# Optimization experiments

Hardware: AMD Instinct MI355X
Metric: run time of the kernel (lower is better)

## Reference

```python
import jax, jax.numpy as jnp
import numpy as np
from jax import lax

B, S = 256, 512
CHAR_NUM, CLASS_NUM, OUTPUT_NUM, WORD_EMBED, H = 10, 10, 64, 32, 128
EPS = 1e-12


def setup_inputs() -> dict:
    key = jax.random.key(0)
    ks = jax.random.split(key, 16)
    def nrm(k, shape, s=0.05):
        return jax.random.normal(k, shape, dtype=jnp.float32) * s
    return {
        "char_ids": jax.random.randint(ks[0], (B, S), 0, CHAR_NUM),
        "word_ids": jax.random.randint(ks[1], (B, S), 0, CHAR_NUM),
        "subject_ids": jax.random.randint(ks[2], (B, 2), 0, S),
        "emb_char": nrm(ks[3], (CHAR_NUM, OUTPUT_NUM)),
        "emb_word": nrm(ks[4], (CHAR_NUM, WORD_EMBED)),
        "Wwc": nrm(ks[5], (WORD_EMBED, OUTPUT_NUM)),
        "bwc": jnp.zeros((OUTPUT_NUM,), jnp.float32),
        "l1_Wx": nrm(ks[6], (OUTPUT_NUM, 4 * H)),
        "l1_Wh": nrm(ks[7], (H, 4 * H)),
        "l1_b": jnp.zeros((4 * H,), jnp.float32),
        "l2_Wx": nrm(ks[8], (H, 4 * H)),
        "l2_Wh": nrm(ks[9], (H, 4 * H)),
        "l2_b": jnp.zeros((4 * H,), jnp.float32),
        "beta_W": nrm(ks[10], (2 * H, H)),
        "beta_b": jnp.zeros((H,), jnp.float32),
        "gamma_W": nrm(ks[11], (2 * H, H)),
        "gamma_b": jnp.zeros((H,), jnp.float32),
        "sub_W": nrm(ks[12], (H, 2)),
        "sub_b": jnp.zeros((2,), jnp.float32),
        "po_W": nrm(ks[13], (H, 2 * CLASS_NUM)),
        "po_b": jnp.zeros((2 * CLASS_NUM,), jnp.float32),
    }


def _lstm_cell(x, h, c, Wx, Wh, b):
    # Keras LSTMCell: gates ordered i, f, g(cell), o
    z = x @ Wx + h @ Wh + b
    i, f, g, o = jnp.split(z, 4, axis=-1)
    c_new = jax.nn.sigmoid(f) * c + jax.nn.sigmoid(i) * jnp.tanh(g)
    h_new = jax.nn.sigmoid(o) * jnp.tanh(c_new)
    return h_new, c_new


def reference(char_ids, word_ids, subject_ids,
              emb_char, emb_word, Wwc, bwc,
              l1_Wx, l1_Wh, l1_b, l2_Wx, l2_Wh, l2_b,
              beta_W, beta_b, gamma_W, gamma_b,
              sub_W, sub_b, po_W, po_b):
    b, s = char_ids.shape
    # NOTE: source passes mask = (char_ids == 0) to the RNN; in Keras, mask True
    # means the step IS processed, so only positions with id==0 update state.
    step_mask = (char_ids == 0)  # [B, S] bool

    emb = emb_char[char_ids] + (emb_word[word_ids] @ Wwc + bwc)  # [B, S, 64]

    def step(carry, inp):
        h1, c1, h2, c2 = carry
        xt, mt = inp  # xt [B, 64], mt [B]
        h1n, c1n = _lstm_cell(xt, h1, c1, l1_Wx, l1_Wh, l1_b)
        h2n, c2n = _lstm_cell(h1n, h2, c2, l2_Wx, l2_Wh, l2_b)
        m = mt[:, None]
        h1 = jnp.where(m, h1n, h1)
        c1 = jnp.where(m, c1n, c1)
        h2 = jnp.where(m, h2n, h2)
        c2 = jnp.where(m, c2n, c2)
        return (h1, c1, h2, c2), h2

    z = jnp.zeros((b, H), emb.dtype)
    _, outs = lax.scan(step, (z, z, z, z),
                       (emb.transpose(1, 0, 2), step_mask.T))
    sent = outs.transpose(1, 0, 2)  # [B, S, 128]

    # vectorized batch_gather (replaces eager numpy per-row loop)
    bidx = jnp.arange(b)
    sub_start = sent[bidx, subject_ids[:, 0]]  # [B, 128]
    sub_end = sent[bidx, subject_ids[:, 1]]    # [B, 128]
    subject = jnp.concatenate([sub_start, sub_end], axis=1)  # [B, 256]

    # conditional layer norm
    beta = subject @ beta_W + beta_b    # [B, 128]
    gamma = subject @ gamma_W + gamma_b
    u = jnp.mean(sent, axis=-1, keepdims=True)
    v = jnp.mean((sent - u) ** 2, axis=-1, keepdims=True)
    xhat = (sent - u) / jnp.sqrt(v + EPS)
    context = gamma[:, None, :] * xhat + beta[:, None, :]  # [B, S, 128]

    # (transformer_encoder LSTM(32) output is dead code in the source; omitted)
    sub_preds = sent @ sub_W + sub_b                     # [B, S, 2]
    po_preds = (context @ po_W + po_b).reshape(b, -1, CLASS_NUM, 2)  # [B, S, 10, 2]
    return sub_preds, po_preds
```

## Files before the change

kernel.cpp:

```cpp
#include <hip/hip_runtime.h>
#include <cstdint>
#include <cstddef>


#define HIST 128
#define HPAD 132

typedef _Float16 f16x2 __attribute__((ext_vector_type(2)));

__device__ __forceinline__ f16x2 as_h2(unsigned int v) {
    union { unsigned int u; f16x2 h; } x; x.u = v; return x.h;
}

#if __has_builtin(__builtin_amdgcn_fdot2)
__device__ __forceinline__ float fdot2(f16x2 a, f16x2 b, float c) {
    return __builtin_amdgcn_fdot2(a, b, c, false);
}
#else
__device__ __forceinline__ float fdot2(f16x2 a, f16x2 b, float c) {
    return c + (float)a.x * (float)b.x + (float)a.y * (float)b.y;
}
#endif

__device__ __forceinline__ float fast_rcp(float x) {
#if __has_builtin(__builtin_amdgcn_rcpf)
    return __builtin_amdgcn_rcpf(x);
#else
    return 1.f / x;
#endif
}
__device__ __forceinline__ float sigm(float x) {
    x = fminf(fmaxf(x, -30.f), 30.f);
    return fast_rcp(1.f + __expf(-x));
}
__device__ __forceinline__ float tanh_fast(float x) {
    x = fminf(fmaxf(x, -15.f), 15.f);
    float e = __expf(-2.f * x);
    return (1.f - e) * fast_rcp(1.f + e);
}

__device__ __forceinline__ float dpp_bfly4(float v) {
    union { float f; int i; } a, b;
    a.f = v;
    b.i = __builtin_amdgcn_update_dpp(0, a.i, 0xB1, 0xf, 0xf, true);
    a.f += b.f;
    b.i = __builtin_amdgcn_update_dpp(0, a.i, 0x4E, 0xf, 0xf, true);
    a.f += b.f;
    return a.f;
}

__device__ __forceinline__ float dot_u4(float s, const uint4 h, const uint4 w) {
    s = fdot2(as_h2(h.x), as_h2(w.x), s);
    s = fdot2(as_h2(h.y), as_h2(w.y), s);
    s = fdot2(as_h2(h.z), as_h2(w.z), s);
    s = fdot2(as_h2(h.w), as_h2(w.w), s);
    return s;
}

__global__ __launch_bounds__(512) void k_prep(
    const float* __restrict__ emb_char, const float* __restrict__ emb_word,
    const float* __restrict__ Wwc, const float* __restrict__ bwc,
    const float* __restrict__ l1_Wx, const float* __restrict__ l1_b,
    const float* __restrict__ l1_Wh, const float* __restrict__ l2_Wx,
    const float* __restrict__ l2_Wh,
    float* __restrict__ XW1, uint4* __restrict__ W1H, uint4* __restrict__ W2H)
{
    const int blk = blockIdx.x;
    const int T = threadIdx.x;
    if (blk < 10) {
        __shared__ float xw[64];
        if (T < 64) {
            float acc = emb_char[T] + bwc[T];
            for (int m = 0; m < 32; ++m) acc += emb_word[blk * 32 + m] * Wwc[m * 64 + T];
            xw[T] = acc;
        }
        __syncthreads();
        float acc = l1_b[T];
        for (int k = 0; k < 64; ++k) acc += xw[k] * l1_Wx[k * 512 + T];
        XW1[blk * 512 + T] = acc;
    } else {
        const int gid = (blk - 10) * 512 + T;
        union { uint4 qv; f16x2 h[4]; } out;
        if (gid < 8192) {
            const int t = gid >> 4, i = gid & 15;
            const int q = t & 3, u = t >> 2;
            const int j = i >> 2, m = i & 3;
            const int col = u + 128 * j;
            for (int e = 0; e < 4; ++e) {
                const int k = 32 * q + 2 * (4 * m + e);
                f16x2 p;
                p.x = (_Float16)l1_Wh[k * 512 + col];
                p.y = (_Float16)l1_Wh[(k + 1) * 512 + col];
                out.h[e] = p;
            }
            W1H[gid] = out.qv;
        } else {
            const int gid2 = gid - 8192;
            const int t = gid2 >> 5, i = gid2 & 31;
            const int q = t & 3, u = t >> 2;
            const int ph = i >> 4, jm = i & 15;
            const int j = jm >> 2, m = jm & 3;
            const int col = u + 128 * j;
            const float* __restrict__ src = ph ? l2_Wx : l2_Wh;
            for (int e = 0; e < 4; ++e) {
                const int k = 32 * q + 2 * (4 * m + e);
                f16x2 p;
                p.x = (_Float16)src[k * 512 + col];
                p.y = (_Float16)src[(k + 1) * 512 + col];
                out.h[e] = p;
            }
            W2H[gid2] = out.qv;
        }
    }
}

__global__ __launch_bounds__(512, 2) void k_lstm(
    const int* __restrict__ char_ids, const int* __restrict__ word_ids,
    const int* __restrict__ subject_ids,
    const float* __restrict__ XW1, const uint4* __restrict__ W1H,
    const uint4* __restrict__ W2H, const float* __restrict__ l2_b,
    const float* __restrict__ beta_W, const float* __restrict__ beta_b,
    const float* __restrict__ gamma_W, const float* __restrict__ gamma_b,
    const float* __restrict__ sub_W, const float* __restrict__ sub_b,
    const float* __restrict__ po_W, const float* __restrict__ po_b,
    float* __restrict__ out)
{
    const int b    = blockIdx.x;
    const int T    = threadIdx.x;
    const int lane = T & 63;
    const int wv   = T >> 6;
    const int q    = T & 3;
    const int u    = T >> 2;

    __shared__ int   charL[512];
    __shared__ int   wordL[512];
    __shared__ float XW1L[5120];
    __shared__ __align__(16) _Float16 h1f[2][128];
    __shared__ __align__(16) _Float16 h2f[2][128];
    __shared__ short actT[512];
    __shared__ short wlist[512];
    __shared__ unsigned short idxL[512];
    __shared__ int   ccnt[8];
    __shared__ __align__(16) float hl[HIST * HPAD];
    __shared__ float A[20][132];
    __shared__ float K1[20], K2[20];
    __shared__ float gm[128], bt[128];
    __shared__ float urs[HIST][2];
    __shared__ float povals[HIST * 20];
    __shared__ float subv[HIST * 2];
    __shared__ float swl[256];
    __shared__ float subj[256];

    charL[T] = char_ids[b * 512 + T];
    wordL[T] = word_ids[b * 512 + T];
#pragma unroll
    for (int i = 0; i < 10; ++i) XW1L[i * 512 + T] = XW1[i * 512 + T];
    __syncthreads();

    const bool act = (charL[T] == 0);
    const unsigned long long bmask = __ballot(act);
    if (lane == 0) ccnt[wv] = (int)__popcll(bmask);
    __syncthreads();
    int base = 0;
    for (int i = 0; i < wv; ++i) base += ccnt[i];
    int tot = base;
    for (int i = wv; i < 8; ++i) tot += ccnt[i];
    if (act) {
        const int pos = base + (int)__popcll(bmask & ((1ull << lane) - 1ull));
        actT[pos]  = (short)T;
        wlist[pos] = (short)wordL[T];
    }
    {
        const int cin = base + (int)__popcll(bmask & ((2ull << lane) - 1ull));
        idxL[T] = (unsigned short)(cin < HIST - 1 ? cin : HIST - 1);
    }
    const int nact = tot;

    if (T < 128) {
        h1f[0][T] = (_Float16)0.f;
        h1f[1][T] = (_Float16)0.f;
        h2f[0][T] = (_Float16)0.f;
        h2f[1][T] = (_Float16)0.f;
        hl[T]     = 0.f;
    }
    float c1 = 0.f, c2 = 0.f;
    const float l2b0 = l2_b[u];
    const float l2b1 = l2_b[128 + u];
    const float l2b2 = l2_b[256 + u];
    const float l2b3 = l2_b[384 + u];

    uint4 w1[16], w2[32];
    {
        const uint4* W1t = W1H + (size_t)T * 16;
        const uint4* W2t = W2H + (size_t)T * 32;
#pragma unroll
        for (int i = 0; i < 16; ++i) w1[i] = W1t[i];
#pragma unroll
        for (int i = 0; i < 32; ++i) w2[i] = W2t[i];
    }
#pragma unroll
    for (int i = 0; i < 16; ++i)
        asm volatile("" : "+v"(w1[i].x), "+v"(w1[i].y), "+v"(w1[i].z), "+v"(w1[i].w));
#pragma unroll
    for (int i = 0; i < 32; ++i)
        asm volatile("" : "+v"(w2[i].x), "+v"(w2[i].y), "+v"(w2[i].z), "+v"(w2[i].w));

    __syncthreads();

    if (nact > 0) {
        const int w0_ = wlist[0];
        const float zi = XW1L[w0_ * 512 + u];
        const float zg = XW1L[w0_ * 512 + 256 + u];
        const float zo = XW1L[w0_ * 512 + 384 + u];
        c1 = sigm(zi) * tanh_fast(zg);
        const float h1n = sigm(zo) * tanh_fast(c1);
        if (q == 0) h1f[0][u] = (_Float16)h1n;
        __syncthreads();
    }

#define LSTM_STEP(H1S, H2S, H1D, H2D)                                          \
    {                                                                          \
        const uint4* h1r = (const uint4*)&H1S[0] + 4 * q;                      \
        const uint4 a0 = h1r[0], a1 = h1r[1], a2 = h1r[2], a3 = h1r[3];        \
        const uint4* h2r = (const uint4*)&H2S[0] + 4 * q;                      \
        const uint4 g0 = h2r[0], g1 = h2r[1], g2 = h2r[2], g3 = h2r[3];        \
        const bool more = (a + 1 < nact);                                      \
        const int wid = more ? wlist[a + 1] : 0;                               \
        const float xwi = XW1L[wid * 512 + u];                                 \
        const float xwf = XW1L[wid * 512 + 128 + u];                           \
        const float xwg = XW1L[wid * 512 + 256 + u];                           \
        const float xwo = XW1L[wid * 512 + 384 + u];                           \
        float p[4];                                                            \
        _Pragma("unroll")                                                      \
        for (int j = 0; j < 4; ++j) {                                          \
            float s = dot_u4(0.f, g0, w2[4 * j + 0]);                          \
            s = dot_u4(s, g1, w2[4 * j + 1]);                                  \
            s = dot_u4(s, g2, w2[4 * j + 2]);                                  \
            s = dot_u4(s, g3, w2[4 * j + 3]);                                  \
            s = dot_u4(s, a0, w2[16 + 4 * j + 0]);                             \
            s = dot_u4(s, a1, w2[16 + 4 * j + 1]);                             \
            s = dot_u4(s, a2, w2[16 + 4 * j + 2]);                             \
            s = dot_u4(s, a3, w2[16 + 4 * j + 3]);                             \
            p[j] = s;                                                          \
        }                                                                      \
        const float y0 = dpp_bfly4(p[0]) + l2b0;                               \
        const float y1 = dpp_bfly4(p[1]) + l2b1;                               \
        const float y2 = dpp_bfly4(p[2]) + l2b2;                               \
        const float y3 = dpp_bfly4(p[3]) + l2b3;                               \
        c2 = sigm(y1) * c2 + sigm(y0) * tanh_fast(y2);                         \
        const float h2v = sigm(y3) * tanh_fast(c2);                            \
        if (q == 0) {                                                          \
            H2D[u] = (_Float16)h2v;                                            \
            const int slot = (a + 1 < HIST - 1) ? a + 1 : HIST - 1;            \
            hl[slot * HPAD + u] = h2v;                                         \
        }                                                                      \
        if (more) {                                                            \
            float r0, r1, r2, r3;                                              \
            {                                                                  \
                float r = dot_u4(0.f, a0, w1[0]);                              \
                r = dot_u4(r, a1, w1[1]);                                      \
                r = dot_u4(r, a2, w1[2]);                                      \
                r = dot_u4(r, a3, w1[3]);                                      \
                r0 = r;                                                        \
                r = dot_u4(0.f, a0, w1[4]);                                    \
                r = dot_u4(r, a1, w1[5]);                                      \
                r = dot_u4(r, a2, w1[6]);                                      \
                r = dot_u4(r, a3, w1[7]);                                      \
                r1 = r;                                                        \
                r = dot_u4(0.f, a0, w1[8]);                                    \
                r = dot_u4(r, a1, w1[9]);                                      \
                r = dot_u4(r, a2, w1[10]);                                     \
                r = dot_u4(r, a3, w1[11]);                                     \
                r2 = r;                                                        \
                r = dot_u4(0.f, a0, w1[12]);                                   \
                r = dot_u4(r, a1, w1[13]);                                     \
                r = dot_u4(r, a2, w1[14]);                                     \
                r = dot_u4(r, a3, w1[15]);                                     \
                r3 = r;                                                        \
            }                                                                  \
            const float zi = dpp_bfly4(r0) + xwi;                              \
            const float zf = dpp_bfly4(r1) + xwf;                              \
            const float zg = dpp_bfly4(r2) + xwg;                              \
            const float zo = dpp_bfly4(r3) + xwo;                              \
            c1 = sigm(zf) * c1 + sigm(zi) * tanh_fast(zg);                     \
            const float h1n = sigm(zo) * tanh_fast(c1);                        \
            if (q == 0) H1D[u] = (_Float16)h1n;                                \
        }                                                                      \
        __syncthreads();                                                       \
    }

    int a = 0;
    while (a < nact) {
        LSTM_STEP(h1f[0], h2f[0], h1f[1], h2f[1]);
        ++a;
        if (a >= nact) break;
        LSTM_STEP(h1f[1], h2f[1], h1f[0], h2f[0]);
        ++a;
    }
#undef LSTM_STEP

    if (T < 256) {
        swl[T] = sub_W[T];
        const int uu = T & 127, half = T >> 7;
        const int sidx = subject_ids[b * 2 + half];
        const int slot = idxL[sidx];
        subj[T] = hl[slot * HPAD + uu];
    }
    __syncthreads();

    if (T < 256) {
        const int uu = T & 127, half = T >> 7;
        const float* __restrict__ W = half ? gamma_W : beta_W;
        float acc = half ? gamma_b[uu] : beta_b[uu];
        for (int c = 0; c < 256; ++c) acc += subj[c] * W[c * 128 + uu];
        if (half) gm[uu] = acc;
        else      bt[uu] = acc;
    }
    __syncthreads();

    for (int i = T; i < 2560; i += 512) {
        const int o = i >> 7, c = i & 127;
        A[o][c] = gm[c] * po_W[c * 20 + o];
    }
    if (T < 20) {
        float k1 = po_b[T], k2 = 0.f;
        for (int c = 0; c < 128; ++c) {
            const float pw = po_W[c * 20 + T];
            k1 += bt[c] * pw;
            k2 += gm[c] * pw;
        }
        K1[T] = k1; K2[T] = k2;
    }
    const int nslot = (int)idxL[511] + 1;
    const float sb0 = sub_b[0], sb1 = sub_b[1];
    for (int s = T; s < nslot; s += 512) {
        const float4* hp4 = (const float4*)&hl[s * HPAD];
        float sum = 0.f, s2 = 0.f, sub0 = sb0, sub1 = sb1;
        for (int c4 = 0; c4 < 32; ++c4) {
            const float4 h = hp4[c4];
            sum += (h.x + h.y) + (h.z + h.w);
            s2  += h.x * h.x + h.y * h.y + h.z * h.z + h.w * h.w;
            const int c = 4 * c4;
            sub0 += h.x * swl[2 * c] + h.y * swl[2 * c + 2] + h.z * swl[2 * c + 4] + h.w * swl[2 * c + 6];
            sub1 += h.x * swl[2 * c + 1] + h.y * swl[2 * c + 3] + h.z * swl[2 * c + 5] + h.w * swl[2 * c + 7];
        }
        const float mu = sum * (1.f / 128.f);
        const float vv = fmaxf(s2 * (1.f / 128.f) - mu * mu, 0.f);
        urs[s][0] = mu;
        urs[s][1] = 1.f / sqrtf(vv + 1e-12f);
        subv[2 * s] = sub0; subv[2 * s + 1] = sub1;
    }
    __syncthreads();

    for (int i = T; i < nslot * 20; i += 512) {
        const int s = i / 20, o = i - 20 * s;
        const float mu = urs[s][0], rs = urs[s][1];
        const float4* hp4 = (const float4*)&hl[s * HPAD];
        const float* Ao = &A[o][0];
        float acc = 0.f;
        for (int c4 = 0; c4 < 32; ++c4) {
            const float4 h = hp4[c4];
            const float4 aa = *(const float4*)&Ao[4 * c4];
            acc += h.x * aa.x + h.y * aa.y + h.z * aa.z + h.w * aa.w;
        }
        povals[i] = rs * acc - mu * rs * K2[o] + K1[o];
    }
    __syncthreads();

    for (int i = T; i < 2560; i += 512) {
        const int t = i / 5, j = i - 5 * t;
        const int sl = idxL[t];
        const float4 v = *(const float4*)&povals[sl * 20 + 4 * j];
        *(float4*)&out[262144 + ((size_t)(b * 512 + t)) * 20 + 4 * j] = v;
    }
    for (int i = T; i < 512; i += 512) {
        const int sl = idxL[i];
        float2 v; v.x = subv[2 * sl]; v.y = subv[2 * sl + 1];
        *(float2*)&out[((size_t)(b * 512 + i)) * 2] = v;
    }
}

extern "C" void kernel_launch(void* const* d_in, const int* in_sizes, int n_in,
                              void* d_out, int out_size, void* d_ws, size_t ws_size,
                              hipStream_t stream) {
    (void)in_sizes; (void)n_in; (void)out_size; (void)ws_size;
    const int*   char_ids    = (const int*)d_in[0];
    const int*   word_ids    = (const int*)d_in[1];
    const int*   subject_ids = (const int*)d_in[2];
    const float* emb_char    = (const float*)d_in[3];
    const float* emb_word    = (const float*)d_in[4];
    const float* Wwc         = (const float*)d_in[5];
    const float* bwc         = (const float*)d_in[6];
    const float* l1_Wx       = (const float*)d_in[7];
    const float* l1_Wh       = (const float*)d_in[8];
    const float* l1_b        = (const float*)d_in[9];
    const float* l2_Wx       = (const float*)d_in[10];
    const float* l2_Wh       = (const float*)d_in[11];
    const float* l2_b        = (const float*)d_in[12];
    const float* beta_W      = (const float*)d_in[13];
    const float* beta_b      = (const float*)d_in[14];
    const float* gamma_W     = (const float*)d_in[15];
    const float* gamma_b     = (const float*)d_in[16];
    const float* sub_W       = (const float*)d_in[17];
    const float* sub_b       = (const float*)d_in[18];
    const float* po_W        = (const float*)d_in[19];
    const float* po_b        = (const float*)d_in[20];
    float* out = (float*)d_out;

    char* ws = (char*)d_ws;
    float* XW1 = (float*)(ws + 0);
    uint4* W1H = (uint4*)(ws + 32768);
    uint4* W2H = (uint4*)(ws + 163840);

    k_prep<<<dim3(58), dim3(512), 0, stream>>>(emb_char, emb_word, Wwc, bwc,
                                               l1_Wx, l1_b, l1_Wh, l2_Wx, l2_Wh,
                                               XW1, W1H, W2H);
    k_lstm<<<dim3(256), dim3(512), 0, stream>>>(char_ids, word_ids, subject_ids,
                                                XW1, W1H, W2H, l2_b,
                                                beta_W, beta_b, gamma_W, gamma_b,
                                                sub_W, sub_b, po_W, po_b, out);
}
```

Before: 232.6 us.

## Replace fdot2 LSTM recurrence with MFMA 16x16x32 matvecs using fused h concat

The per-step recurrent matvecs for both LSTM layers now run on MFMA 16x16x32 f16 instructions instead of fdot2 chains plus DPP butterfly reductions. Weights are repacked by the prep kernel into a single per-thread MFMA B-operand layout, and h2/h1 are stored as one concatenated half-precision buffer that feeds the A operand. Only row 0 of each MFMA tile is useful, so most of the matrix work is wasted. Only 16 lanes per wave compute the gate nonlinearities, and each step's MFMA dependency-chain latency may dominate.

```diff
diff --git a/kernel.cpp b/kernel.cpp
--- a/kernel.cpp
+++ b/kernel.cpp
@@ -6,21 +6,14 @@
 #define HIST 128
 #define HPAD 132
 
-typedef _Float16 f16x2 __attribute__((ext_vector_type(2)));
-
-__device__ __forceinline__ f16x2 as_h2(unsigned int v) {
-    union { unsigned int u; f16x2 h; } x; x.u = v; return x.h;
-}
-
-#if __has_builtin(__builtin_amdgcn_fdot2)
-__device__ __forceinline__ float fdot2(f16x2 a, f16x2 b, float c) {
-    return __builtin_amdgcn_fdot2(a, b, c, false);
-}
-#else
-__device__ __forceinline__ float fdot2(f16x2 a, f16x2 b, float c) {
-    return c + (float)a.x * (float)b.x + (float)a.y * (float)b.y;
-}
-#endif
+typedef _Float16 f16x8 __attribute__((ext_vector_type(8)));
+typedef float    f32x4 __attribute__((ext_vector_type(4)));
+
+__device__ __forceinline__ f16x8 as_h8(const uint4& v) {
+    f16x8 r; __builtin_memcpy(&r, &v, 16); return r;
+}
+
+#define MFMA16(a, b, c) __builtin_amdgcn_mfma_f32_16x16x32_f16((a), (b), (c), 0, 0, 0)
 
 __device__ __forceinline__ float fast_rcp(float x) {
 #if __has_builtin(__builtin_amdgcn_rcpf)
@@ -39,31 +32,13 @@
     return (1.f - e) * fast_rcp(1.f + e);
 }
 
-__device__ __forceinline__ float dpp_bfly4(float v) {
-    union { float f; int i; } a, b;
-    a.f = v;
-    b.i = __builtin_amdgcn_update_dpp(0, a.i, 0xB1, 0xf, 0xf, true);
-    a.f += b.f;
-    b.i = __builtin_amdgcn_update_dpp(0, a.i, 0x4E, 0xf, 0xf, true);
-    a.f += b.f;
-    return a.f;
-}
-
-__device__ __forceinline__ float dot_u4(float s, const uint4 h, const uint4 w) {
-    s = fdot2(as_h2(h.x), as_h2(w.x), s);
-    s = fdot2(as_h2(h.y), as_h2(w.y), s);
-    s = fdot2(as_h2(h.z), as_h2(w.z), s);
-    s = fdot2(as_h2(h.w), as_h2(w.w), s);
-    return s;
-}
-
 __global__ __launch_bounds__(512) void k_prep(
     const float* __restrict__ emb_char, const float* __restrict__ emb_word,
     const float* __restrict__ Wwc, const float* __restrict__ bwc,
     const float* __restrict__ l1_Wx, const float* __restrict__ l1_b,
     const float* __restrict__ l1_Wh, const float* __restrict__ l2_Wx,
     const float* __restrict__ l2_Wh,
-    float* __restrict__ XW1, uint4* __restrict__ W1H, uint4* __restrict__ W2H)
+    float* __restrict__ XW1, uint4* __restrict__ WF)
 {
     const int blk = blockIdx.x;
     const int T = threadIdx.x;
@@ -80,45 +55,32 @@
         XW1[blk * 512 + T] = acc;
     } else {
         const int gid = (blk - 10) * 512 + T;
-        union { uint4 qv; f16x2 h[4]; } out;
-        if (gid < 8192) {
-            const int t = gid >> 4, i = gid & 15;
-            const int q = t & 3, u = t >> 2;
-            const int j = i >> 2, m = i & 3;
-            const int col = u + 128 * j;
-            for (int e = 0; e < 4; ++e) {
-                const int k = 32 * q + 2 * (4 * m + e);
-                f16x2 p;
-                p.x = (_Float16)l1_Wh[k * 512 + col];
-                p.y = (_Float16)l1_Wh[(k + 1) * 512 + col];
-                out.h[e] = p;
-            }
-            W1H[gid] = out.qv;
-        } else {
-            const int gid2 = gid - 8192;
-            const int t = gid2 >> 5, i = gid2 & 31;
-            const int q = t & 3, u = t >> 2;
-            const int ph = i >> 4, jm = i & 15;
-            const int j = jm >> 2, m = jm & 3;
-            const int col = u + 128 * j;
-            const float* __restrict__ src = ph ? l2_Wx : l2_Wh;
-            for (int e = 0; e < 4; ++e) {
-                const int k = 32 * q + 2 * (4 * m + e);
-                f16x2 p;
-                p.x = (_Float16)src[k * 512 + col];
-                p.y = (_Float16)src[(k + 1) * 512 + col];
-                out.h[e] = p;
-            }
-            W2H[gid2] = out.qv;
-        }
+        const int thr = gid / 48;
+        const int f   = gid - thr * 48;
+        const int w   = thr >> 6, l = thr & 63;
+        const int kb  = 8 * (l >> 4);
+        const bool isL2 = (f < 32);
+        int j, ks;
+        if (isL2) { j = f >> 3; ks = f & 7; }
+        else      { const int f2 = f - 32; j = f2 >> 2; ks = f2 & 3; }
+        const int col = j * 128 + 16 * w + (l & 15);
+        union { uint4 qv; _Float16 h[8]; } o;
+        for (int e = 0; e < 8; ++e) {
+            const int k = ks * 32 + kb + e;
+            float v;
+            if (isL2) v = (k < 128) ? l2_Wh[k * 512 + col] : l2_Wx[(k - 128) * 512 + col];
+            else      v = l1_Wh[k * 512 + col];
+            o.h[e] = (_Float16)v;
+        }
+        WF[gid] = o.qv;
     }
 }
 
 __global__ __launch_bounds__(512, 2) void k_lstm(
     const int* __restrict__ char_ids, const int* __restrict__ word_ids,
     const int* __restrict__ subject_ids,
-    const float* __restrict__ XW1, const uint4* __restrict__ W1H,
-    const uint4* __restrict__ W2H, const float* __restrict__ l2_b,
+    const float* __restrict__ XW1, const uint4* __restrict__ WF,
+    const float* __restrict__ l2_b,
     const float* __restrict__ beta_W, const float* __restrict__ beta_b,
     const float* __restrict__ gamma_W, const float* __restrict__ gamma_b,
     const float* __restrict__ sub_W, const float* __restrict__ sub_b,
@@ -129,15 +91,14 @@
     const int T    = threadIdx.x;
     const int lane = T & 63;
     const int wv   = T >> 6;
-    const int q    = T & 3;
-    const int u    = T >> 2;
+    const int kb   = 8 * (lane >> 4);
+    const int unit = 16 * wv + (lane & 15);
+    const bool g16 = (lane < 16);
 
     __shared__ int   charL[512];
     __shared__ int   wordL[512];
     __shared__ float XW1L[5120];
-    __shared__ __align__(16) _Float16 h1f[2][128];
-    __shared__ __align__(16) _Float16 h2f[2][128];
-    __shared__ short actT[512];
+    __shared__ __align__(16) _Float16 hcat[2][256];
     __shared__ short wlist[512];
     __shared__ unsigned short idxL[512];
     __shared__ int   ccnt[8];
@@ -167,7 +128,6 @@
     for (int i = wv; i < 8; ++i) tot += ccnt[i];
     if (act) {
         const int pos = base + (int)__popcll(bmask & ((1ull << lane) - 1ull));
-        actT[pos]  = (short)T;
         wlist[pos] = (short)wordL[T];
     }
     {
@@ -177,127 +137,82 @@
     const int nact = tot;
 
     if (T < 128) {
-        h1f[0][T] = (_Float16)0.f;
-        h1f[1][T] = (_Float16)0.f;
-        h2f[0][T] = (_Float16)0.f;
-        h2f[1][T] = (_Float16)0.f;
-        hl[T]     = 0.f;
+        hcat[0][T] = (_Float16)0.f;
+        hl[T]      = 0.f;
     }
     float c1 = 0.f, c2 = 0.f;
-    const float l2b0 = l2_b[u];
-    const float l2b1 = l2_b[128 + u];
-    const float l2b2 = l2_b[256 + u];
-    const float l2b3 = l2_b[384 + u];
-
-    uint4 w1[16], w2[32];
+    const float l2b0 = l2_b[unit];
+    const float l2b1 = l2_b[128 + unit];
+    const float l2b2 = l2_b[256 + unit];
+    const float l2b3 = l2_b[384 + unit];
+
+    uint4 wf[48];
     {
-        const uint4* W1t = W1H + (size_t)T * 16;
-        const uint4* W2t = W2H + (size_t)T * 32;
+        const uint4* p = WF + (size_t)T * 48;
 #pragma unroll
-        for (int i = 0; i < 16; ++i) w1[i] = W1t[i];
-#pragma unroll
-        for (int i = 0; i < 32; ++i) w2[i] = W2t[i];
-    }
-#pragma unroll
-    for (int i = 0; i < 16; ++i)
-        asm volatile("" : "+v"(w1[i].x), "+v"(w1[i].y), "+v"(w1[i].z), "+v"(w1[i].w));
-#pragma unroll
-    for (int i = 0; i < 32; ++i)
-        asm volatile("" : "+v"(w2[i].x), "+v"(w2[i].y), "+v"(w2[i].z), "+v"(w2[i].w));
-
+        for (int i = 0; i < 48; ++i) wf[i] = p[i];
+    }
     __syncthreads();
 
     if (nact > 0) {
         const int w0_ = wlist[0];
-        const float zi = XW1L[w0_ * 512 + u];
-        const float zg = XW1L[w0_ * 512 + 256 + u];
-        const float zo = XW1L[w0_ * 512 + 384 + u];
+        const float zi = XW1L[w0_ * 512 + unit];
+        const float zg = XW1L[w0_ * 512 + 256 + unit];
+        const float zo = XW1L[w0_ * 512 + 384 + unit];
         c1 = sigm(zi) * tanh_fast(zg);
         const float h1n = sigm(zo) * tanh_fast(c1);
-        if (q == 0) h1f[0][u] = (_Float16)h1n;
+        if (g16) hcat[0][128 + unit] = (_Float16)h1n;
         __syncthreads();
     }
 
-#define LSTM_STEP(H1S, H2S, H1D, H2D)                                          \
-    {                                                                          \
-        const uint4* h1r = (const uint4*)&H1S[0] + 4 * q;                      \
-        const uint4 a0 = h1r[0], a1 = h1r[1], a2 = h1r[2], a3 = h1r[3];        \
-        const uint4* h2r = (const uint4*)&H2S[0] + 4 * q;                      \
-        const uint4 g0 = h2r[0], g1 = h2r[1], g2 = h2r[2], g3 = h2r[3];        \
-        const bool more = (a + 1 < nact);                                      \
-        const int wid = more ? wlist[a + 1] : 0;                               \
-        const float xwi = XW1L[wid * 512 + u];                                 \
-        const float xwf = XW1L[wid * 512 + 128 + u];                           \
-        const float xwg = XW1L[wid * 512 + 256 + u];                           \
-        const float xwo = XW1L[wid * 512 + 384 + u];                           \
-        float p[4];                                                            \
-        _Pragma("unroll")                                                      \
-        for (int j = 0; j < 4; ++j) {                                          \
-            float s = dot_u4(0.f, g0, w2[4 * j + 0]);                          \
-            s = dot_u4(s, g1, w2[4 * j + 1]);                                  \
-            s = dot_u4(s, g2, w2[4 * j + 2]);                                  \
-            s = dot_u4(s, g3, w2[4 * j + 3]);                                  \
-            s = dot_u4(s, a0, w2[16 + 4 * j + 0]);                             \
-            s = dot_u4(s, a1, w2[16 + 4 * j + 1]);                             \
-            s = dot_u4(s, a2, w2[16 + 4 * j + 2]);                             \
-            s = dot_u4(s, a3, w2[16 + 4 * j + 3]);                             \
-            p[j] = s;                                                          \
-        }                                                                      \
-        const float y0 = dpp_bfly4(p[0]) + l2b0;                               \
-        const float y1 = dpp_bfly4(p[1]) + l2b1;                               \
-        const float y2 = dpp_bfly4(p[2]) + l2b2;                               \
-        const float y3 = dpp_bfly4(p[3]) + l2b3;                               \
-        c2 = sigm(y1) * c2 + sigm(y0) * tanh_fast(y2);                         \
-        const float h2v = sigm(y3) * tanh_fast(c2);                            \
-        if (q == 0) {                                                          \
-            H2D[u] = (_Float16)h2v;                                            \
-            const int slot = (a + 1 < HIST - 1) ? a + 1 : HIST - 1;            \
-            hl[slot * HPAD + u] = h2v;                                         \
-        }                                                                      \
-        if (more) {                                                            \
-            float r0, r1, r2, r3;                                              \
-            {                                                                  \
-                float r = dot_u4(0.f, a0, w1[0]);                              \
-                r = dot_u4(r, a1, w1[1]);                                      \
-                r = dot_u4(r, a2, w1[2]);                                      \
-                r = dot_u4(r, a3, w1[3]);                                      \
-                r0 = r;                                                        \
-                r = dot_u4(0.f, a0, w1[4]);                                    \
-                r = dot_u4(r, a1, w1[5]);                                      \
-                r = dot_u4(r, a2, w1[6]);                                      \
-                r = dot_u4(r, a3, w1[7]);                                      \
-                r1 = r;                                                        \
-                r = dot_u4(0.f, a0, w1[8]);                                    \
-                r = dot_u4(r, a1, w1[9]);                                      \
-                r = dot_u4(r, a2, w1[10]);                                     \
-                r = dot_u4(r, a3, w1[11]);                                     \
-                r2 = r;                                                        \
-                r = dot_u4(0.f, a0, w1[12]);                                   \
-                r = dot_u4(r, a1, w1[13]);                                     \
-                r = dot_u4(r, a2, w1[14]);                                     \
-                r = dot_u4(r, a3, w1[15]);                                     \
-                r3 = r;                                                        \
-            }                                                                  \
-            const float zi = dpp_bfly4(r0) + xwi;                              \
-            const float zf = dpp_bfly4(r1) + xwf;                              \
-            const float zg = dpp_bfly4(r2) + xwg;                              \
-            const float zo = dpp_bfly4(r3) + xwo;                              \
-            c1 = sigm(zf) * c1 + sigm(zi) * tanh_fast(zg);                     \
-            const float h1n = sigm(zo) * tanh_fast(c1);                        \
-            if (q == 0) H1D[u] = (_Float16)h1n;                                \
-        }                                                                      \
-        __syncthreads();                                                       \
-    }
-
-    int a = 0;
-    while (a < nact) {
-        LSTM_STEP(h1f[0], h2f[0], h1f[1], h2f[1]);
-        ++a;
-        if (a >= nact) break;
-        LSTM_STEP(h1f[1], h2f[1], h1f[0], h2f[0]);
-        ++a;
-    }
-#undef LSTM_STEP
+    int cur = 0;
+    for (int a = 0; a < nact; ++a) {
+        const _Float16* hc = hcat[cur];
+        _Float16*       hn = hcat[cur ^ 1];
+
+        f32x4 acc0 = {l2b0, 0.f, 0.f, 0.f};
+        f32x4 acc1 = {l2b1, 0.f, 0.f, 0.f};
+        f32x4 acc2 = {l2b2, 0.f, 0.f, 0.f};
+        f32x4 acc3 = {l2b3, 0.f, 0.f, 0.f};
+#pragma unroll
+        for (int ks = 0; ks < 8; ++ks) {
+            const f16x8 aa = *(const f16x8*)&hc[kb + 32 * ks];
+            acc0 = MFMA16(aa, as_h8(wf[0 * 8 + ks]), acc0);
+            acc1 = MFMA16(aa, as_h8(wf[1 * 8 + ks]), acc1);
+            acc2 = MFMA16(aa, as_h8(wf[2 * 8 + ks]), acc2);
+            acc3 = MFMA16(aa, as_h8(wf[3 * 8 + ks]), acc3);
+        }
+        if (g16) {
+            c2 = sigm(acc1[0]) * c2 + sigm(acc0[0]) * tanh_fast(acc2[0]);
+            const float h2v = sigm(acc3[0]) * tanh_fast(c2);
+            hn[unit] = (_Float16)h2v;
+            const int slot = (a + 1 < HIST - 1) ? a + 1 : HIST - 1;
+            hl[slot * HPAD + unit] = h2v;
+        }
+
+        if (a + 1 < nact) {
+            const int wid = wlist[a + 1];
+            f32x4 r0 = {XW1L[wid * 512 + unit],       0.f, 0.f, 0.f};
+            f32x4 r1 = {XW1L[wid * 512 + 128 + unit], 0.f, 0.f, 0.f};
+            f32x4 r2 = {XW1L[wid * 512 + 256 + unit], 0.f, 0.f, 0.f};
+            f32x4 r3 = {XW1L[wid * 512 + 384 + unit], 0.f, 0.f, 0.f};
+#pragma unroll
+            for (int ks = 0; ks < 4; ++ks) {
+                const f16x8 aa = *(const f16x8*)&hc[128 + kb + 32 * ks];
+                r0 = MFMA16(aa, as_h8(wf[32 + 0 * 4 + ks]), r0);
+                r1 = MFMA16(aa, as_h8(wf[32 + 1 * 4 + ks]), r1);
+                r2 = MFMA16(aa, as_h8(wf[32 + 2 * 4 + ks]), r2);
+                r3 = MFMA16(aa, as_h8(wf[32 + 3 * 4 + ks]), r3);
+            }
+            if (g16) {
+                c1 = sigm(r1[0]) * c1 + sigm(r0[0]) * tanh_fast(r2[0]);
+                const float h1n = sigm(r3[0]) * tanh_fast(c1);
+                hn[128 + unit] = (_Float16)h1n;
+            }
+        }
+        __syncthreads();
+        cur ^= 1;
+    }
 
     if (T < 256) {
         swl[T] = sub_W[T];
@@ -392,8 +307,8 @@
     const float* Wwc         = (const float*)d_in[5];
     const float* bwc         = (const float*)d_in[6];
     const float* l1_Wx       = (const float*)d_in[7];
+    const float* l1_b        = (const float*)d_in[9];
     const float* l1_Wh       = (const float*)d_in[8];
-    const float* l1_b        = (const float*)d_in[9];
     const float* l2_Wx       = (const float*)d_in[10];
     const float* l2_Wh       = (const float*)d_in[11];
     const float* l2_b        = (const float*)d_in[12];
@@ -409,14 +324,13 @@
 
     char* ws = (char*)d_ws;
     float* XW1 = (float*)(ws + 0);
-    uint4* W1H = (uint4*)(ws + 32768);
-    uint4* W2H = (uint4*)(ws + 163840);
+    uint4* WF  = (uint4*)(ws + 32768);
 
     k_prep<<<dim3(58), dim3(512), 0, stream>>>(emb_char, emb_word, Wwc, bwc,
                                                l1_Wx, l1_b, l1_Wh, l2_Wx, l2_Wh,
-                                               XW1, W1H, W2H);
+                                               XW1, WF);
     k_lstm<<<dim3(256), dim3(512), 0, stream>>>(char_ids, word_ids, subject_ids,
-                                                XW1, W1H, W2H, l2_b,
+                                                XW1, WF, l2_b,
                                                 beta_W, beta_b, gamma_W, gamma_b,
                                                 sub_W, sub_b, po_W, po_b, out);
 }
```

Measured after the change: 203.3 us. 12.6% less time.
